# Performance work log

Hardware: AMD Instinct MI355X
Metric: run time of the kernel (lower is better)

The kernel has to match this reference:

```python
import jax, jax.numpy as jnp
import numpy as np

NUM_BINS = 15
NUM_CLASSES = 4
NEIGHBORHOOD_WIDTH = 3  # K; num_neighbor_classes = K**2 = 9


def _neighbor_counts(onehot):
    """Count of same-class neighbors in KxK window (center excluded), zero padding.
    onehot: [B, C, H, W] float32 one-hot of hard predictions.
    returns int32 [B, C, H, W] in [0, K^2-1].
    """
    K = NEIGHBORHOOD_WIDTH
    C = onehot.shape[1]
    kern = np.ones((K, K), dtype=np.float32)
    kern[K // 2, K // 2] = 0.0  # exclude center pixel
    kernel = jnp.asarray(np.broadcast_to(kern, (C, 1, K, K)).copy())  # depthwise OIHW
    counts = jax.lax.conv_general_dilated(
        onehot, kernel,
        window_strides=(1, 1), padding='SAME',
        feature_group_count=C,
        dimension_numbers=('NCHW', 'OIHW', 'NCHW'))
    return jnp.clip(jnp.round(counts).astype(jnp.int32), 0, K * K - 1)


def setup_inputs() -> dict:
    key = jax.random.key(0)
    k1, k2 = jax.random.split(key)
    logits = jax.random.normal(k1, (16, NUM_CLASSES, 512, 512), dtype=jnp.float32)
    # calibration frequency table: val_freqs[class][neighbor_count][conf_bin]
    val_freqs = jax.random.uniform(k2, (NUM_CLASSES, NEIGHBORHOOD_WIDTH ** 2, NUM_BINS), dtype=jnp.float32)
    return {"logits": logits, "val_freqs": val_freqs}


def reference(logits, val_freqs):
    B, C, H, W = logits.shape
    probs = jax.nn.softmax(logits, axis=1)                      # [B,C,H,W]
    y_hard = jnp.argmax(probs, axis=1)                          # [B,H,W]

    # (y_hard == lab_idx) for every class at once -> one-hot [B,C,H,W]
    onehot = jax.nn.one_hot(y_hard, C, axis=1, dtype=jnp.float32)
    agg = _neighbor_counts(onehot)                              # [B,C,H,W] int32 in [0, K^2-1]

    # confidence bin per pixel/class: uniform bins on [0,1]
    bin_width = 1.0 / NUM_BINS
    bin_map = jnp.clip((probs / bin_width).astype(jnp.int32), 0, NUM_BINS - 1)  # [B,C,H,W]

    # fused multi-index gather replacing the nested class/neighbor-mask loops:
    # calibrated[b,c,h,w] = val_freqs[c, agg[b,c,h,w], bin_map[b,c,h,w]]
    cls_idx = jnp.arange(C, dtype=jnp.int32)[None, :, None, None]
    calibrated = val_freqs[cls_idx, agg, bin_map]               # [B,C,H,W]

    # normalize across classes, guarding zero sums
    s = jnp.sum(calibrated, axis=1, keepdims=True)
    s = jnp.where(s == 0, 1.0, s)
    return calibrated / s
```

## Files before the change

### kernel.cpp

```cpp
#include <hip/hip_runtime.h>

#define HW (512 * 512)

typedef float vfloat4 __attribute__((ext_vector_type(4)));

constexpr int TX = 64, TY = 16;
constexpr int CWP = 67;
constexpr float BWIDTH = 1.0f / 15.0f;
constexpr float DELTA = 3e-5f;

__global__ __launch_bounds__(256) void nectar_binning_kernel(
    const float* __restrict__ logits,
    const float* __restrict__ val_freqs,
    float* __restrict__ out)
{
    __shared__ unsigned int cls[18 * CWP];
    __shared__ float vf[540];

    const int b  = blockIdx.z;
    const int w0 = blockIdx.x * TX;
    const int h0 = blockIdx.y * TY;
    const int tid = threadIdx.x;

    for (int i = tid; i < 540; i += 256) vf[i] = val_freqs[i];

    const float* lb = logits + (size_t)b * 4 * HW;

    const int tix = tid & 15;
    const int tiy = tid >> 4;
    const int w = w0 + 4 * tix;
    const int h = h0 + tiy;
    const int base = (h << 9) + w;

    float xv[4][4];
    #pragma unroll
    for (int c = 0; c < 4; c++) {
        vfloat4 v = *reinterpret_cast<const vfloat4*>(lb + (size_t)c * HW + base);
        xv[c][0] = v.x; xv[c][1] = v.y; xv[c][2] = v.z; xv[c][3] = v.w;
    }

    unsigned int pbin[4];
    #pragma unroll
    for (int j = 0; j < 4; j++) {
        float x0 = xv[0][j], x1 = xv[1][j], x2 = xv[2][j], x3 = xv[3][j];
        int c = 0; float best = x0;
        if (x1 > best) { best = x1; c = 1; }
        if (x2 > best) { best = x2; c = 2; }
        if (x3 > best) { best = x3; c = 3; }
        cls[(tiy + 1) * CWP + 1 + 4 * tix + j] = 1u << (4 * c);

        float m = fmaxf(fmaxf(x0, x1), fmaxf(x2, x3));
        float t0 = x0 - m, t1 = x1 - m, t2 = x2 - m, t3 = x3 - m;
        float f0 = __expf(t0), f1 = __expf(t1), f2 = __expf(t2), f3 = __expf(t3);
        float sf = ((f0 + f1) + f2) + f3;
        float rs = __builtin_amdgcn_rcpf(sf);
        float q[4];
        q[0] = (f0 * rs) * 15.0f; q[1] = (f1 * rs) * 15.0f;
        q[2] = (f2 * rs) * 15.0f; q[3] = (f3 * rs) * 15.0f;
        bool slow = false;
        #pragma unroll
        for (int c2 = 0; c2 < 4; c2++) {
            float fr = q[c2] - floorf(q[c2]);
            slow |= (fr < DELTA) | (fr > 1.0f - DELTA);
        }
        if (slow) {
            float e0 = expf(t0), e1 = expf(t1), e2 = expf(t2), e3 = expf(t3);
            float s = ((e0 + e1) + e2) + e3;
            q[0] = (e0 / s) / BWIDTH; q[1] = (e1 / s) / BWIDTH;
            q[2] = (e2 / s) / BWIDTH; q[3] = (e3 / s) / BWIDTH;
        }
        unsigned int pb = 0;
        #pragma unroll
        for (int c2 = 0; c2 < 4; c2++) {
            int bin = (int)q[c2];
            bin = bin > 14 ? 14 : bin;
            pb |= (unsigned int)bin << (4 * c2);
        }
        pbin[j] = pb;
    }

    if (tid < 164) {
        int ly, lx;
        if (tid < 66)       { ly = 0;        lx = tid;       }
        else if (tid < 132) { ly = 17;       lx = tid - 66;  }
        else if (tid < 148) { ly = tid - 131; lx = 0;        }
        else                { ly = tid - 147; lx = 65;       }
        int hh = h0 + ly - 1;
        int ww = w0 + lx - 1;
        unsigned int v = 0;
        if ((unsigned)hh < 512u && (unsigned)ww < 512u) {
            int bb = (hh << 9) + ww;
            float x0 = lb[bb];
            float x1 = lb[HW + bb];
            float x2 = lb[2 * HW + bb];
            float x3 = lb[3 * HW + bb];
            int c = 0; float best = x0;
            if (x1 > best) { best = x1; c = 1; }
            if (x2 > best) { best = x2; c = 2; }
            if (x3 > best) { best = x3; c = 3; }
            v = 1u << (4 * c);
        }
        cls[ly * CWP + lx] = v;
    }
    __syncthreads();

    const unsigned int* p0 = &cls[tiy * CWP + 4 * tix];
    unsigned int r1[6], colsum[6];
    #pragma unroll
    for (int j = 0; j < 6; j++) {
        unsigned int a = p0[j];
        unsigned int bmid = p0[CWP + j];
        unsigned int cbot = p0[2 * CWP + j];
        r1[j] = bmid;
        colsum[j] = a + bmid + cbot;
    }

    float res[4][4];
    #pragma unroll
    for (int j = 0; j < 4; j++) {
        unsigned int pk = colsum[j] + colsum[j + 1] + colsum[j + 2] - r1[j + 1];
        unsigned int pb = pbin[j];
        float cs = 0.0f;
        float cal[4];
        #pragma unroll
        for (int c = 0; c < 4; c++) {
            int cnt = (int)((pk >> (4 * c)) & 0xFu);
            int bin = (int)((pb >> (4 * c)) & 0xFu);
            float v = vf[c * 135 + cnt * 15 + bin];
            cal[c] = v;
            cs += v;
        }
        if (cs == 0.0f) cs = 1.0f;
        float inv = __builtin_amdgcn_rcpf(cs);
        #pragma unroll
        for (int c = 0; c < 4; c++) res[c][j] = cal[c] * inv;
    }

    float* ob = out + (size_t)b * 4 * HW + base;
    #pragma unroll
    for (int c = 0; c < 4; c++) {
        vfloat4 v;
        v.x = res[c][0]; v.y = res[c][1]; v.z = res[c][2]; v.w = res[c][3];
        __builtin_nontemporal_store(v, reinterpret_cast<vfloat4*>(ob + (size_t)c * HW));
    }
}

extern "C" void kernel_launch(void* const* d_in, const int* in_sizes, int n_in,
                              void* d_out, int out_size, void* d_ws, size_t ws_size,
                              hipStream_t stream) {
    const float* logits    = (const float*)d_in[0];
    const float* val_freqs = (const float*)d_in[1];
    float* out             = (float*)d_out;

    dim3 block(256, 1, 1);
    dim3 grid(512 / TX, 512 / TY, 16);
    hipLaunchKernelGGL(nectar_binning_kernel, grid, block, 0, stream,
                       logits, val_freqs, out);
}
```

Measured before the change: 118.2 us.

## Double tile height to 32 rows with 8 pixels per thread and hoisted halo loads

Doubles the tile height so each thread handles 8 pixels with two vec4 loads per class. This halves the relative halo overhead and block count. The halo ring loads are moved ahead of the softmax/binning loop so their latency can overlap compute. The bin extraction reuses the int cast instead of floorf. The cost is higher register pressure from the larger per-thread arrays, which may lower occupancy.

```diff
diff --git a/kernel.cpp b/kernel.cpp
--- a/kernel.cpp
+++ b/kernel.cpp
@@ -4,7 +4,7 @@
 
 typedef float vfloat4 __attribute__((ext_vector_type(4)));
 
-constexpr int TX = 64, TY = 16;
+constexpr int TX = 64, TY = 32;
 constexpr int CWP = 67;
 constexpr float BWIDTH = 1.0f / 15.0f;
 constexpr float DELTA = 3e-5f;
@@ -14,7 +14,7 @@
     const float* __restrict__ val_freqs,
     float* __restrict__ out)
 {
-    __shared__ unsigned int cls[18 * CWP];
+    __shared__ unsigned int cls[34 * CWP];
     __shared__ float vf[540];
 
     const int b  = blockIdx.z;
@@ -26,68 +26,31 @@
 
     const float* lb = logits + (size_t)b * 4 * HW;
 
-    const int tix = tid & 15;
-    const int tiy = tid >> 4;
-    const int w = w0 + 4 * tix;
+    const int tix = tid & 7;
+    const int tiy = tid >> 3;
+    const int w = w0 + 8 * tix;
     const int h = h0 + tiy;
     const int base = (h << 9) + w;
 
-    float xv[4][4];
+    float xv[4][8];
     #pragma unroll
     for (int c = 0; c < 4; c++) {
-        vfloat4 v = *reinterpret_cast<const vfloat4*>(lb + (size_t)c * HW + base);
-        xv[c][0] = v.x; xv[c][1] = v.y; xv[c][2] = v.z; xv[c][3] = v.w;
+        vfloat4 v0 = *reinterpret_cast<const vfloat4*>(lb + (size_t)c * HW + base);
+        vfloat4 v1 = *reinterpret_cast<const vfloat4*>(lb + (size_t)c * HW + base + 4);
+        xv[c][0] = v0.x; xv[c][1] = v0.y; xv[c][2] = v0.z; xv[c][3] = v0.w;
+        xv[c][4] = v1.x; xv[c][5] = v1.y; xv[c][6] = v1.z; xv[c][7] = v1.w;
     }
 
-    unsigned int pbin[4];
-    #pragma unroll
-    for (int j = 0; j < 4; j++) {
-        float x0 = xv[0][j], x1 = xv[1][j], x2 = xv[2][j], x3 = xv[3][j];
-        int c = 0; float best = x0;
-        if (x1 > best) { best = x1; c = 1; }
-        if (x2 > best) { best = x2; c = 2; }
-        if (x3 > best) { best = x3; c = 3; }
-        cls[(tiy + 1) * CWP + 1 + 4 * tix + j] = 1u << (4 * c);
-
-        float m = fmaxf(fmaxf(x0, x1), fmaxf(x2, x3));
-        float t0 = x0 - m, t1 = x1 - m, t2 = x2 - m, t3 = x3 - m;
-        float f0 = __expf(t0), f1 = __expf(t1), f2 = __expf(t2), f3 = __expf(t3);
-        float sf = ((f0 + f1) + f2) + f3;
-        float rs = __builtin_amdgcn_rcpf(sf);
-        float q[4];
-        q[0] = (f0 * rs) * 15.0f; q[1] = (f1 * rs) * 15.0f;
-        q[2] = (f2 * rs) * 15.0f; q[3] = (f3 * rs) * 15.0f;
-        bool slow = false;
-        #pragma unroll
-        for (int c2 = 0; c2 < 4; c2++) {
-            float fr = q[c2] - floorf(q[c2]);
-            slow |= (fr < DELTA) | (fr > 1.0f - DELTA);
-        }
-        if (slow) {
-            float e0 = expf(t0), e1 = expf(t1), e2 = expf(t2), e3 = expf(t3);
-            float s = ((e0 + e1) + e2) + e3;
-            q[0] = (e0 / s) / BWIDTH; q[1] = (e1 / s) / BWIDTH;
-            q[2] = (e2 / s) / BWIDTH; q[3] = (e3 / s) / BWIDTH;
-        }
-        unsigned int pb = 0;
-        #pragma unroll
-        for (int c2 = 0; c2 < 4; c2++) {
-            int bin = (int)q[c2];
-            bin = bin > 14 ? 14 : bin;
-            pb |= (unsigned int)bin << (4 * c2);
-        }
-        pbin[j] = pb;
-    }
-
-    if (tid < 164) {
-        int ly, lx;
-        if (tid < 66)       { ly = 0;        lx = tid;       }
-        else if (tid < 132) { ly = 17;       lx = tid - 66;  }
-        else if (tid < 148) { ly = tid - 131; lx = 0;        }
-        else                { ly = tid - 147; lx = 65;       }
-        int hh = h0 + ly - 1;
-        int ww = w0 + lx - 1;
-        unsigned int v = 0;
+    bool ring = tid < 196;
+    int rly, rlx;
+    if (tid < 66)       { rly = 0;         rlx = tid;       }
+    else if (tid < 132) { rly = 33;        rlx = tid - 66;  }
+    else if (tid < 164) { rly = tid - 131; rlx = 0;         }
+    else                { rly = tid - 163; rlx = 65;        }
+    unsigned int rv = 0;
+    if (ring) {
+        int hh = h0 + rly - 1;
+        int ww = w0 + rlx - 1;
         if ((unsigned)hh < 512u && (unsigned)ww < 512u) {
             int bb = (hh << 9) + ww;
             float x0 = lb[bb];
@@ -98,26 +61,67 @@
             if (x1 > best) { best = x1; c = 1; }
             if (x2 > best) { best = x2; c = 2; }
             if (x3 > best) { best = x3; c = 3; }
-            v = 1u << (4 * c);
+            rv = 1u << (4 * c);
         }
-        cls[ly * CWP + lx] = v;
+        cls[rly * CWP + rlx] = rv;
+    }
+
+    unsigned int pbin[8];
+    #pragma unroll
+    for (int j = 0; j < 8; j++) {
+        float x0 = xv[0][j], x1 = xv[1][j], x2 = xv[2][j], x3 = xv[3][j];
+        int c = 0; float best = x0;
+        if (x1 > best) { best = x1; c = 1; }
+        if (x2 > best) { best = x2; c = 2; }
+        if (x3 > best) { best = x3; c = 3; }
+        cls[(tiy + 1) * CWP + 1 + 8 * tix + j] = 1u << (4 * c);
+
+        float m = fmaxf(fmaxf(x0, x1), fmaxf(x2, x3));
+        float t0 = x0 - m, t1 = x1 - m, t2 = x2 - m, t3 = x3 - m;
+        float f0 = __expf(t0), f1 = __expf(t1), f2 = __expf(t2), f3 = __expf(t3);
+        float sf = ((f0 + f1) + f2) + f3;
+        float rs = __builtin_amdgcn_rcpf(sf);
+        float q[4];
+        q[0] = (f0 * rs) * 15.0f; q[1] = (f1 * rs) * 15.0f;
+        q[2] = (f2 * rs) * 15.0f; q[3] = (f3 * rs) * 15.0f;
+        int bin[4];
+        bool slow = false;
+        #pragma unroll
+        for (int c2 = 0; c2 < 4; c2++) {
+            bin[c2] = (int)q[c2];
+            float fr = q[c2] - (float)bin[c2];
+            slow |= (fr < DELTA) | (fr > 1.0f - DELTA);
+        }
+        if (slow) {
+            float e0 = expf(t0), e1 = expf(t1), e2 = expf(t2), e3 = expf(t3);
+            float s = ((e0 + e1) + e2) + e3;
+            bin[0] = (int)((e0 / s) / BWIDTH); bin[1] = (int)((e1 / s) / BWIDTH);
+            bin[2] = (int)((e2 / s) / BWIDTH); bin[3] = (int)((e3 / s) / BWIDTH);
+        }
+        unsigned int pb = 0;
+        #pragma unroll
+        for (int c2 = 0; c2 < 4; c2++) {
+            int bc = bin[c2] > 14 ? 14 : bin[c2];
+            pb |= (unsigned int)bc << (4 * c2);
+        }
+        pbin[j] = pb;
     }
     __syncthreads();
 
-    const unsigned int* p0 = &cls[tiy * CWP + 4 * tix];
-    unsigned int r1[6], colsum[6];
+    const unsigned int* p0 = &cls[tiy * CWP + 8 * tix];
+    unsigned int r1[10], colsum[10];
     #pragma unroll
-    for (int j = 0; j < 6; j++) {
-        unsigned int a = p0[j];
+    for (int j = 0; j < 10; j++) {
+        unsigned int a    = p0[j];
         unsigned int bmid = p0[CWP + j];
         unsigned int cbot = p0[2 * CWP + j];
         r1[j] = bmid;
         colsum[j] = a + bmid + cbot;
     }
 
-    float res[4][4];
+    float res[4][8];
     #pragma unroll
-    for (int j = 0; j < 4; j++) {
+    for (int j = 0; j < 8; j++) {
         unsigned int pk = colsum[j] + colsum[j + 1] + colsum[j + 2] - r1[j + 1];
         unsigned int pb = pbin[j];
         float cs = 0.0f;
@@ -139,9 +143,11 @@
     float* ob = out + (size_t)b * 4 * HW + base;
     #pragma unroll
     for (int c = 0; c < 4; c++) {
-        vfloat4 v;
-        v.x = res[c][0]; v.y = res[c][1]; v.z = res[c][2]; v.w = res[c][3];
-        __builtin_nontemporal_store(v, reinterpret_cast<vfloat4*>(ob + (size_t)c * HW));
+        vfloat4 v0, v1;
+        v0.x = res[c][0]; v0.y = res[c][1]; v0.z = res[c][2]; v0.w = res[c][3];
+        v1.x = res[c][4]; v1.y = res[c][5]; v1.z = res[c][6]; v1.w = res[c][7];
+        __builtin_nontemporal_store(v0, reinterpret_cast<vfloat4*>(ob + (size_t)c * HW));
+        __builtin_nontemporal_store(v1, reinterpret_cast<vfloat4*>(ob + (size_t)c * HW + 4));
     }
 }
 
```

New measurement: 122.8 us. +3.8%, slower.

## Split fused kernel into classify/bin pass and stencil-gather pass via workspace

Applied to the files above, without the earlier changes.

Replaces the single fused kernel with two kernels. The first computes argmax and confidence bins per pixel and packs them into one 32-bit word written to workspace. The second reads the packed words with a halo from global memory and does the neighbor count, table gather and normalization. This removes the halo recomputation and shared-memory stencil from the logits pass, at the cost of an extra 16 MB write and read of the packed intermediate plus a second launch. The old fused kernel is kept as a fallback for when the workspace is too small.

```diff
diff --git a/kernel.cpp b/kernel.cpp
--- a/kernel.cpp
+++ b/kernel.cpp
@@ -3,42 +3,165 @@
 #define HW (512 * 512)
 
 typedef float vfloat4 __attribute__((ext_vector_type(4)));
-
-constexpr int TX = 64, TY = 16;
-constexpr int CWP = 67;
+typedef unsigned int vuint4 __attribute__((ext_vector_type(4)));
+
 constexpr float BWIDTH = 1.0f / 15.0f;
 constexpr float DELTA = 3e-5f;
 
-__global__ __launch_bounds__(256) void nectar_binning_kernel(
-    const float* __restrict__ logits,
-    const float* __restrict__ val_freqs,
+__global__ __launch_bounds__(256) void k1_classbins(
+    const float* __restrict__ logits, unsigned int* __restrict__ packed)
+{
+    const int g  = (blockIdx.x * 256 + threadIdx.x) * 4;
+    const int b  = g >> 18;
+    const int hw = g & (HW - 1);
+    const float* lb = logits + (size_t)b * 4 * HW + hw;
+
+    vfloat4 v[4];
+    #pragma unroll
+    for (int c = 0; c < 4; c++)
+        v[c] = *reinterpret_cast<const vfloat4*>(lb + (size_t)c * HW);
+
+    vuint4 outw;
+    #pragma unroll
+    for (int j = 0; j < 4; j++) {
+        float x0 = v[0][j], x1 = v[1][j], x2 = v[2][j], x3 = v[3][j];
+        int c = 0; float best = x0;
+        if (x1 > best) { best = x1; c = 1; }
+        if (x2 > best) { best = x2; c = 2; }
+        if (x3 > best) { best = x3; c = 3; }
+
+        float m = fmaxf(fmaxf(x0, x1), fmaxf(x2, x3));
+        float t0 = x0 - m, t1 = x1 - m, t2 = x2 - m, t3 = x3 - m;
+        float f0 = __expf(t0), f1 = __expf(t1), f2 = __expf(t2), f3 = __expf(t3);
+        float sf = ((f0 + f1) + f2) + f3;
+        float rs = __builtin_amdgcn_rcpf(sf);
+        float q[4] = { (f0 * rs) * 15.0f, (f1 * rs) * 15.0f,
+                       (f2 * rs) * 15.0f, (f3 * rs) * 15.0f };
+        int bin[4];
+        bool slow = false;
+        #pragma unroll
+        for (int c2 = 0; c2 < 4; c2++) {
+            bin[c2] = (int)q[c2];
+            float fr = q[c2] - (float)bin[c2];
+            slow |= (fr < DELTA) | (fr > 1.0f - DELTA);
+        }
+        if (slow) {
+            float e0 = expf(t0), e1 = expf(t1), e2 = expf(t2), e3 = expf(t3);
+            float s = ((e0 + e1) + e2) + e3;
+            bin[0] = (int)((e0 / s) / BWIDTH); bin[1] = (int)((e1 / s) / BWIDTH);
+            bin[2] = (int)((e2 / s) / BWIDTH); bin[3] = (int)((e3 / s) / BWIDTH);
+        }
+        unsigned int wv = 1u << (16 + 4 * c);
+        #pragma unroll
+        for (int c2 = 0; c2 < 4; c2++) {
+            int bc = bin[c2] > 14 ? 14 : bin[c2];
+            wv |= (unsigned int)bc << (4 * c2);
+        }
+        outw[j] = wv;
+    }
+    *reinterpret_cast<vuint4*>(packed + g) = outw;
+}
+
+__global__ __launch_bounds__(256) void k2_gather(
+    const unsigned int* __restrict__ packed, const float* __restrict__ val_freqs,
+    float* __restrict__ out)
+{
+    __shared__ float vf[540];
+    const int tid = threadIdx.x;
+    for (int i = tid; i < 540; i += 256) vf[i] = val_freqs[i];
+    __syncthreads();
+
+    const int b  = blockIdx.z;
+    const int y0 = blockIdx.x * 4;
+    const int x  = (tid & 127) * 4;
+    const int r  = y0 + (tid >> 7) * 2;
+
+    const unsigned int* pb = packed + (size_t)b * HW;
+
+    unsigned int cell[4][6];
+    #pragma unroll
+    for (int k = 0; k < 4; k++) {
+        int rr = r - 1 + k;
+        if ((unsigned)rr < 512u) {
+            const unsigned int* rp = pb + (rr << 9) + x;
+            vuint4 vv = *reinterpret_cast<const vuint4*>(rp);
+            cell[k][1] = vv.x; cell[k][2] = vv.y; cell[k][3] = vv.z; cell[k][4] = vv.w;
+            cell[k][0] = (x == 0)   ? 0u : rp[-1];
+            cell[k][5] = (x == 508) ? 0u : rp[4];
+        } else {
+            #pragma unroll
+            for (int j = 0; j < 6; j++) cell[k][j] = 0u;
+        }
+    }
+
+    unsigned int colsum[2][6];
+    #pragma unroll
+    for (int j = 0; j < 6; j++) {
+        unsigned int a0 = cell[0][j] >> 16, a1 = cell[1][j] >> 16;
+        unsigned int a2 = cell[2][j] >> 16, a3 = cell[3][j] >> 16;
+        unsigned int mid = a1 + a2;
+        colsum[0][j] = mid + a0;
+        colsum[1][j] = mid + a3;
+    }
+
+    float* ob = out + (size_t)b * 4 * HW;
+    #pragma unroll
+    for (int k = 0; k < 2; k++) {
+        float resv[4][4];
+        #pragma unroll
+        for (int j = 0; j < 4; j++) {
+            unsigned int own = cell[k + 1][j + 1];
+            unsigned int pk  = colsum[k][j] + colsum[k][j + 1] + colsum[k][j + 2]
+                             - (own >> 16);
+            float cs = 0.0f;
+            float cal[4];
+            #pragma unroll
+            for (int c = 0; c < 4; c++) {
+                int cnt = (int)((pk  >> (4 * c)) & 0xFu);
+                int bin = (int)((own >> (4 * c)) & 0xFu);
+                float vv = vf[c * 135 + cnt * 15 + bin];
+                cal[c] = vv;
+                cs += vv;
+            }
+            if (cs == 0.0f) cs = 1.0f;
+            float inv = __builtin_amdgcn_rcpf(cs);
+            #pragma unroll
+            for (int c = 0; c < 4; c++) resv[c][j] = cal[c] * inv;
+        }
+        int basew = ((r + k) << 9) + x;
+        #pragma unroll
+        for (int c = 0; c < 4; c++) {
+            vfloat4 vo;
+            vo.x = resv[c][0]; vo.y = resv[c][1]; vo.z = resv[c][2]; vo.w = resv[c][3];
+            __builtin_nontemporal_store(vo, reinterpret_cast<vfloat4*>(ob + (size_t)c * HW + basew));
+        }
+    }
+}
+
+constexpr int FTX = 64, FTY = 16;
+constexpr int CWP = 67;
+
+__global__ __launch_bounds__(256) void fused_fallback(
+    const float* __restrict__ logits, const float* __restrict__ val_freqs,
     float* __restrict__ out)
 {
     __shared__ unsigned int cls[18 * CWP];
     __shared__ float vf[540];
-
     const int b  = blockIdx.z;
-    const int w0 = blockIdx.x * TX;
-    const int h0 = blockIdx.y * TY;
+    const int w0 = blockIdx.x * FTX;
+    const int h0 = blockIdx.y * FTY;
     const int tid = threadIdx.x;
-
     for (int i = tid; i < 540; i += 256) vf[i] = val_freqs[i];
-
     const float* lb = logits + (size_t)b * 4 * HW;
-
-    const int tix = tid & 15;
-    const int tiy = tid >> 4;
-    const int w = w0 + 4 * tix;
-    const int h = h0 + tiy;
+    const int tix = tid & 15, tiy = tid >> 4;
+    const int w = w0 + 4 * tix, h = h0 + tiy;
     const int base = (h << 9) + w;
-
     float xv[4][4];
     #pragma unroll
     for (int c = 0; c < 4; c++) {
         vfloat4 v = *reinterpret_cast<const vfloat4*>(lb + (size_t)c * HW + base);
         xv[c][0] = v.x; xv[c][1] = v.y; xv[c][2] = v.z; xv[c][3] = v.w;
     }
-
     unsigned int pbin[4];
     #pragma unroll
     for (int j = 0; j < 4; j++) {
@@ -48,52 +171,44 @@
         if (x2 > best) { best = x2; c = 2; }
         if (x3 > best) { best = x3; c = 3; }
         cls[(tiy + 1) * CWP + 1 + 4 * tix + j] = 1u << (4 * c);
-
         float m = fmaxf(fmaxf(x0, x1), fmaxf(x2, x3));
         float t0 = x0 - m, t1 = x1 - m, t2 = x2 - m, t3 = x3 - m;
         float f0 = __expf(t0), f1 = __expf(t1), f2 = __expf(t2), f3 = __expf(t3);
         float sf = ((f0 + f1) + f2) + f3;
         float rs = __builtin_amdgcn_rcpf(sf);
-        float q[4];
-        q[0] = (f0 * rs) * 15.0f; q[1] = (f1 * rs) * 15.0f;
-        q[2] = (f2 * rs) * 15.0f; q[3] = (f3 * rs) * 15.0f;
-        bool slow = false;
-        #pragma unroll
-        for (int c2 = 0; c2 < 4; c2++) {
-            float fr = q[c2] - floorf(q[c2]);
+        float q[4] = {(f0*rs)*15.0f,(f1*rs)*15.0f,(f2*rs)*15.0f,(f3*rs)*15.0f};
+        int bin[4]; bool slow = false;
+        #pragma unroll
+        for (int c2 = 0; c2 < 4; c2++) {
+            bin[c2] = (int)q[c2];
+            float fr = q[c2] - (float)bin[c2];
             slow |= (fr < DELTA) | (fr > 1.0f - DELTA);
         }
         if (slow) {
             float e0 = expf(t0), e1 = expf(t1), e2 = expf(t2), e3 = expf(t3);
             float s = ((e0 + e1) + e2) + e3;
-            q[0] = (e0 / s) / BWIDTH; q[1] = (e1 / s) / BWIDTH;
-            q[2] = (e2 / s) / BWIDTH; q[3] = (e3 / s) / BWIDTH;
-        }
-        unsigned int pb = 0;
-        #pragma unroll
-        for (int c2 = 0; c2 < 4; c2++) {
-            int bin = (int)q[c2];
-            bin = bin > 14 ? 14 : bin;
-            pb |= (unsigned int)bin << (4 * c2);
-        }
-        pbin[j] = pb;
-    }
-
+            bin[0]=(int)((e0/s)/BWIDTH); bin[1]=(int)((e1/s)/BWIDTH);
+            bin[2]=(int)((e2/s)/BWIDTH); bin[3]=(int)((e3/s)/BWIDTH);
+        }
+        unsigned int pbv = 0;
+        #pragma unroll
+        for (int c2 = 0; c2 < 4; c2++) {
+            int bc = bin[c2] > 14 ? 14 : bin[c2];
+            pbv |= (unsigned int)bc << (4 * c2);
+        }
+        pbin[j] = pbv;
+    }
     if (tid < 164) {
         int ly, lx;
-        if (tid < 66)       { ly = 0;        lx = tid;       }
-        else if (tid < 132) { ly = 17;       lx = tid - 66;  }
+        if (tid < 66)       { ly = 0;         lx = tid;      }
+        else if (tid < 132) { ly = 17;        lx = tid - 66; }
         else if (tid < 148) { ly = tid - 131; lx = 0;        }
         else                { ly = tid - 147; lx = 65;       }
-        int hh = h0 + ly - 1;
-        int ww = w0 + lx - 1;
+        int hh = h0 + ly - 1, ww = w0 + lx - 1;
         unsigned int v = 0;
         if ((unsigned)hh < 512u && (unsigned)ww < 512u) {
             int bb = (hh << 9) + ww;
-            float x0 = lb[bb];
-            float x1 = lb[HW + bb];
-            float x2 = lb[2 * HW + bb];
-            float x3 = lb[3 * HW + bb];
+            float x0 = lb[bb], x1 = lb[HW + bb], x2 = lb[2*HW + bb], x3 = lb[3*HW + bb];
             int c = 0; float best = x0;
             if (x1 > best) { best = x1; c = 1; }
             if (x2 > best) { best = x2; c = 2; }
@@ -103,39 +218,32 @@
         cls[ly * CWP + lx] = v;
     }
     __syncthreads();
-
     const unsigned int* p0 = &cls[tiy * CWP + 4 * tix];
     unsigned int r1[6], colsum[6];
     #pragma unroll
     for (int j = 0; j < 6; j++) {
-        unsigned int a = p0[j];
-        unsigned int bmid = p0[CWP + j];
-        unsigned int cbot = p0[2 * CWP + j];
+        unsigned int a = p0[j], bmid = p0[CWP + j], cbot = p0[2 * CWP + j];
         r1[j] = bmid;
         colsum[j] = a + bmid + cbot;
     }
-
     float res[4][4];
     #pragma unroll
     for (int j = 0; j < 4; j++) {
         unsigned int pk = colsum[j] + colsum[j + 1] + colsum[j + 2] - r1[j + 1];
-        unsigned int pb = pbin[j];
-        float cs = 0.0f;
-        float cal[4];
+        unsigned int pbv = pbin[j];
+        float cs = 0.0f, cal[4];
         #pragma unroll
         for (int c = 0; c < 4; c++) {
-            int cnt = (int)((pk >> (4 * c)) & 0xFu);
-            int bin = (int)((pb >> (4 * c)) & 0xFu);
+            int cnt = (int)((pk  >> (4 * c)) & 0xFu);
+            int bin = (int)((pbv >> (4 * c)) & 0xFu);
             float v = vf[c * 135 + cnt * 15 + bin];
-            cal[c] = v;
-            cs += v;
+            cal[c] = v; cs += v;
         }
         if (cs == 0.0f) cs = 1.0f;
         float inv = __builtin_amdgcn_rcpf(cs);
         #pragma unroll
         for (int c = 0; c < 4; c++) res[c][j] = cal[c] * inv;
     }
-
     float* ob = out + (size_t)b * 4 * HW + base;
     #pragma unroll
     for (int c = 0; c < 4; c++) {
@@ -152,8 +260,15 @@
     const float* val_freqs = (const float*)d_in[1];
     float* out             = (float*)d_out;
 
-    dim3 block(256, 1, 1);
-    dim3 grid(512 / TX, 512 / TY, 16);
-    hipLaunchKernelGGL(nectar_binning_kernel, grid, block, 0, stream,
-                       logits, val_freqs, out);
-}
+    const size_t need = (size_t)16 * HW * sizeof(unsigned int);
+    if (ws_size >= need) {
+        unsigned int* packed = (unsigned int*)d_ws;
+        hipLaunchKernelGGL(k1_classbins, dim3(16 * HW / 1024, 1, 1), dim3(256, 1, 1),
+                           0, stream, logits, packed);
+        hipLaunchKernelGGL(k2_gather, dim3(128, 1, 16), dim3(256, 1, 1),
+                           0, stream, packed, val_freqs, out);
+    } else {
+        hipLaunchKernelGGL(fused_fallback, dim3(512 / FTX, 512 / FTY, 16), dim3(256, 1, 1),
+                           0, stream, logits, val_freqs, out);
+    }
+}
```

Result: no change. 120.5 us (+1.9%).
